# Optimization experiments

Hardware: AMD Instinct MI355X
Metric: run time of the kernel (lower is better)

## Reference

```python
import jax, jax.numpy as jnp
import numpy as np

TAU = 0.5

def _projection(z, W1, b1, W2, b2):
    h = jax.nn.elu(z @ W1.T + b1)
    return h @ W2.T + b2

def _normalize(x, eps=1e-12):
    n = jnp.linalg.norm(x, axis=1, keepdims=True)
    return x / jnp.maximum(n, eps)

def setup_inputs() -> dict:
    key = jax.random.key(0)
    k = jax.random.split(key, 6)
    N, D, P = 8192, 256, 256
    s = 1.0 / np.sqrt(D)
    return {
        "z1": jax.random.normal(k[0], (N, D), jnp.float32),
        "z2": jax.random.normal(k[1], (N, D), jnp.float32),
        "W1": jax.random.normal(k[2], (P, D), jnp.float32) * s,
        "b1": jnp.zeros((P,), jnp.float32),
        "W2": jax.random.normal(k[3], (D, P), jnp.float32) * s,
        "b2": jnp.zeros((D,), jnp.float32),
    }

def reference(z1, z2, W1, b1, W2, b2):
    h1 = _projection(z1, W1, b1, W2, b2)
    h2 = _projection(z2, W1, b1, W2, b2)
    n1 = _normalize(h1)
    n2 = _normalize(h2)
    f11 = jnp.exp((n1 @ n1.T) / TAU)  # [N,N]
    f22 = jnp.exp((n2 @ n2.T) / TAU)
    f12 = jnp.exp((n1 @ n2.T) / TAU)
    d12 = jnp.diagonal(f12)
    l1 = -jnp.log(d12 / (f11.sum(1) + f12.sum(1) - jnp.diagonal(f11)))
    # sim(h2,h1) = f12.T: diag same, row-sum = column-sum of f12
    l2 = -jnp.log(d12 / (f22.sum(1) + f12.sum(0) - jnp.diagonal(f22)))
    return (l1 + l2) * 0.5
```

## Files before the change

kernel.cpp:

```cpp
#include <hip/hip_runtime.h>
#include <hip/hip_bf16.h>
#include <hip/hip_fp8.h>
#include <stdint.h>

#define Nn 8192
#define TWO_N 16384
#define INV_TAU 2.0f

typedef unsigned short u16;
typedef unsigned char u8;
typedef __bf16 bf16x8 __attribute__((ext_vector_type(8)));
typedef float f32x4 __attribute__((ext_vector_type(4)));
typedef int i32x8 __attribute__((ext_vector_type(8)));

typedef const __attribute__((address_space(1))) void* gas_ptr;
typedef __attribute__((address_space(3))) void* las_ptr;

__device__ __forceinline__ void async_copy16(const void* g, void* l) {
  __builtin_amdgcn_global_load_lds((gas_ptr)g, (las_ptr)l, 16, 0, 0);
}

__global__ __launch_bounds__(256)
void mlp_norm(const float* __restrict__ z1, const float* __restrict__ z2,
              const float* __restrict__ W1, const float* __restrict__ b1,
              const float* __restrict__ W2, const float* __restrict__ b2,
              u8* __restrict__ Mf8, float* __restrict__ snorm,
              float* __restrict__ rsum) {
  __shared__ __bf16 sZ[64 * 64];
  __shared__ __bf16 sW[256 * 64];
  __shared__ __bf16 sH[64 * 256];
  const int bx = blockIdx.x;
  const int i0 = bx * 64;
  const float* Zsrc = (bx < 128) ? (z1 + (size_t)i0 * 256)
                                 : (z2 + (size_t)(i0 - Nn) * 256);
  const int t = threadIdx.x;
  const int lane = t & 63, wave = t >> 6;
  const int wn = wave * 64;
  const int fr = lane >> 4, fc = lane & 15;
  const int sw = fc & 7;

  if (t < 64) rsum[i0 + t] = 0.f;

  f32x4 acc[4][4];
#pragma unroll
  for (int a = 0; a < 4; a++)
#pragma unroll
    for (int b = 0; b < 4; b++) acc[a][b] = (f32x4){0.f, 0.f, 0.f, 0.f};

  for (int k0 = 0; k0 < 256; k0 += 64) {
    __syncthreads();
#pragma unroll
    for (int it = 0; it < 2; ++it) {
      int c = t + 256 * it;
      int row = c >> 3, g = (c & 7) ^ (row & 7);
      const float* s = Zsrc + (size_t)row * 256 + k0 + g * 8;
      float4 a0 = *(const float4*)s, a1 = *(const float4*)(s + 4);
      bf16x8 v = {(__bf16)a0.x, (__bf16)a0.y, (__bf16)a0.z, (__bf16)a0.w,
                  (__bf16)a1.x, (__bf16)a1.y, (__bf16)a1.z, (__bf16)a1.w};
      *(bf16x8*)&sZ[c * 8] = v;
    }
#pragma unroll
    for (int it = 0; it < 8; ++it) {
      int c = t + 256 * it;
      int row = c >> 3, g = (c & 7) ^ (row & 7);
      const float* s = W1 + (size_t)row * 256 + k0 + g * 8;
      float4 a0 = *(const float4*)s, a1 = *(const float4*)(s + 4);
      bf16x8 v = {(__bf16)a0.x, (__bf16)a0.y, (__bf16)a0.z, (__bf16)a0.w,
                  (__bf16)a1.x, (__bf16)a1.y, (__bf16)a1.z, (__bf16)a1.w};
      *(bf16x8*)&sW[c * 8] = v;
    }
    __syncthreads();
#pragma unroll
    for (int ks = 0; ks < 2; ++ks) {
      bf16x8 af[4], bfr[4];
#pragma unroll
      for (int mi = 0; mi < 4; mi++)
        af[mi] = *(const bf16x8*)&sZ[(mi * 16 + fc) * 64 + (((ks * 4 + fr) ^ sw) * 8)];
#pragma unroll
      for (int ni = 0; ni < 4; ni++)
        bfr[ni] = *(const bf16x8*)&sW[(wn + ni * 16 + fc) * 64 + (((ks * 4 + fr) ^ sw) * 8)];
#pragma unroll
      for (int mi = 0; mi < 4; mi++)
#pragma unroll
        for (int ni = 0; ni < 4; ni++)
          acc[mi][ni] = __builtin_amdgcn_mfma_f32_16x16x32_bf16(af[mi], bfr[ni], acc[mi][ni], 0, 0, 0);
    }
  }

  {
    float bv[4];
#pragma unroll
    for (int ni = 0; ni < 4; ni++) bv[ni] = b1[wn + ni * 16 + fc];
#pragma unroll
    for (int mi = 0; mi < 4; mi++)
#pragma unroll
      for (int ni = 0; ni < 4; ni++) {
        int col = wn + ni * 16 + fc;
        int gc = col >> 3;
#pragma unroll
        for (int r = 0; r < 4; r++) {
          int row = mi * 16 + fr * 4 + r;
          float v = acc[mi][ni][r] + bv[ni];
          v = v > 0.f ? v : (__expf(v) - 1.f);
          int pos = (gc & 24) | ((gc & 7) ^ (row & 7));
          sH[row * 256 + pos * 8 + (col & 7)] = (__bf16)v;
          acc[mi][ni][r] = 0.f;
        }
      }
  }

  for (int k0 = 0; k0 < 256; k0 += 64) {
    __syncthreads();
#pragma unroll
    for (int it = 0; it < 8; ++it) {
      int c = t + 256 * it;
      int row = c >> 3, g = (c & 7) ^ (row & 7);
      const float* s = W2 + (size_t)row * 256 + k0 + g * 8;
      float4 a0 = *(const float4*)s, a1 = *(const float4*)(s + 4);
      bf16x8 v = {(__bf16)a0.x, (__bf16)a0.y, (__bf16)a0.z, (__bf16)a0.w,
                  (__bf16)a1.x, (__bf16)a1.y, (__bf16)a1.z, (__bf16)a1.w};
      *(bf16x8*)&sW[c * 8] = v;
    }
    __syncthreads();
    const int kgb = k0 >> 3;
#pragma unroll
    for (int ks = 0; ks < 2; ++ks) {
      bf16x8 af[4], bfr[4];
#pragma unroll
      for (int mi = 0; mi < 4; mi++)
        af[mi] = *(const bf16x8*)&sH[(mi * 16 + fc) * 256 + (kgb + (((ks * 4 + fr) ^ sw))) * 8];
#pragma unroll
      for (int ni = 0; ni < 4; ni++)
        bfr[ni] = *(const bf16x8*)&sW[(wn + ni * 16 + fc) * 64 + (((ks * 4 + fr) ^ sw) * 8)];
#pragma unroll
      for (int mi = 0; mi < 4; mi++)
#pragma unroll
        for (int ni = 0; ni < 4; ni++)
          acc[mi][ni] = __builtin_amdgcn_mfma_f32_16x16x32_bf16(af[mi], bfr[ni], acc[mi][ni], 0, 0, 0);
    }
  }

  float bv[4];
#pragma unroll
  for (int ni = 0; ni < 4; ni++) bv[ni] = b2[wn + ni * 16 + fc];

  __syncthreads();
  float* red = (float*)sZ;
  float* red2 = red + 256;

#pragma unroll
  for (int mi = 0; mi < 4; mi++) {
    float ssq[4] = {0.f, 0.f, 0.f, 0.f};
#pragma unroll
    for (int ni = 0; ni < 4; ni++)
#pragma unroll
      for (int r = 0; r < 4; r++) {
        float v = acc[mi][ni][r] + bv[ni];
        acc[mi][ni][r] = v;
        ssq[r] += v * v;
      }
#pragma unroll
    for (int r = 0; r < 4; r++) {
      float v = ssq[r];
#pragma unroll
      for (int off = 1; off < 16; off <<= 1) v += __shfl_xor(v, off, 16);
      if (fc == 0) red[(mi * 16 + fr * 4 + r) * 4 + wave] = v;
    }
  }
  __syncthreads();

#pragma unroll
  for (int mi = 0; mi < 4; mi++) {
    float ssq2[4] = {0.f, 0.f, 0.f, 0.f};
#pragma unroll
    for (int r = 0; r < 4; r++) {
      int row = mi * 16 + fr * 4 + r;
      float ss = red[row * 4] + red[row * 4 + 1] + red[row * 4 + 2] + red[row * 4 + 3];
      float rn = 1.f / fmaxf(sqrtf(ss), 1e-12f);
#pragma unroll
      for (int ni = 0; ni < 4; ni++) {
        float v = acc[mi][ni][r] * rn;
        __hip_fp8_e4m3 q(v);
        Mf8[(size_t)(i0 + row) * 256 + wn + ni * 16 + fc] = q.__x;
        float fv = (float)q;
        ssq2[r] += fv * fv;
      }
    }
#pragma unroll
    for (int r = 0; r < 4; r++) {
      float v = ssq2[r];
#pragma unroll
      for (int off = 1; off < 16; off <<= 1) v += __shfl_xor(v, off, 16);
      if (fc == 0) red2[(mi * 16 + fr * 4 + r) * 4 + wave] = v;
    }
  }
  __syncthreads();
  if (t < 64)
    snorm[i0 + t] = red2[t * 4] + red2[t * 4 + 1] + red2[t * 4 + 2] + red2[t * 4 + 3];
}

__global__ __launch_bounds__(256, 2)
void gram_sym(const u8* __restrict__ Mf8, float* __restrict__ rsum) {
  __shared__ u8 sB8[2][128 * 256];
  const int t = threadIdx.x;
  const int lane = t & 63, wave = t >> 6;
  const int wm = (wave >> 1) * 64, wn = (wave & 1) * 64;
  const int fr = lane >> 4, fc = lane & 15;

  int f = 2111 - blockIdx.x;
  int b = 0;
  while (f >= 2 * (b + 1) * (b + 2)) ++b;
  int rem = f - 2 * b * (b + 1);
  int r = rem / (b + 1);
  int q = rem - r * (b + 1);
  int k = 4 * b + 1 + r;
  const int i_t = 128 - k;
  const int jt0 = i_t + 4 * q;
  const int L = min(4, k - 4 * q);
  const int i0 = i_t * 128;

  {
    const u8* Bg = Mf8 + (size_t)jt0 * 128 * 256;
#pragma unroll
    for (int it = 0; it < 8; ++it) {
      int c = t + 256 * it;
      int row = c >> 4, slot = c & 15;
      int g = slot ^ (row & 15);
      async_copy16(Bg + (size_t)row * 256 + g * 16, (void*)&sB8[0][c * 16]);
    }
  }

  i32x8 afr[4][2];
  {
    const u8* Ag = Mf8 + (size_t)i0 * 256;
#pragma unroll
    for (int mi = 0; mi < 4; ++mi) {
      const u8* rp = Ag + (size_t)(wm + mi * 16 + fc) * 256 + fr * 32;
#pragma unroll
      for (int kb = 0; kb < 2; ++kb) {
        int4 lo = *(const int4*)(rp + kb * 128);
        int4 hi = *(const int4*)(rp + kb * 128 + 16);
        afr[mi][kb] = (i32x8){lo.x, lo.y, lo.z, lo.w, hi.x, hi.y, hi.z, hi.w};
      }
    }
  }

  float rowacc[4][4];
#pragma unroll
  for (int a = 0; a < 4; a++)
#pragma unroll
    for (int rr = 0; rr < 4; rr++) rowacc[a][rr] = 0.f;

  for (int jt = 0; jt < L; ++jt) {
    const int j_t = jt0 + jt;
    const int j0 = j_t * 128;
    const u8* sB = &sB8[jt & 1][0];

    __syncthreads();

    if (jt + 1 < L) {
      const u8* Bg = Mf8 + (size_t)(j_t + 1) * 128 * 256;
      u8* dst = &sB8[(jt + 1) & 1][0];
#pragma unroll
      for (int it = 0; it < 8; ++it) {
        int c = t + 256 * it;
        int row = c >> 4, slot = c & 15;
        int g = slot ^ (row & 15);
        async_copy16(Bg + (size_t)row * 256 + g * 16, (void*)&dst[c * 16]);
      }
    }

    f32x4 acc[4][4];
#pragma unroll
    for (int a = 0; a < 4; a++)
#pragma unroll
      for (int bb = 0; bb < 4; bb++) acc[a][bb] = (f32x4){0.f, 0.f, 0.f, 0.f};

#pragma unroll
    for (int kb = 0; kb < 2; ++kb) {
      i32x8 bfrag[4];
#pragma unroll
      for (int ni = 0; ni < 4; ++ni) {
        const u8* base = sB + (wn + ni * 16 + fc) * 256;
        int g0 = kb * 8 + fr * 2;
        int4 lo = *(const int4*)(base + ((g0 ^ fc) * 16));
        int4 hi = *(const int4*)(base + (((g0 + 1) ^ fc) * 16));
        bfrag[ni] = (i32x8){lo.x, lo.y, lo.z, lo.w, hi.x, hi.y, hi.z, hi.w};
      }
#pragma unroll
      for (int mi = 0; mi < 4; mi++)
#pragma unroll
        for (int ni = 0; ni < 4; ni++)
          acc[mi][ni] = __builtin_amdgcn_mfma_scale_f32_16x16x128_f8f6f4(
              afr[mi][kb], bfrag[ni], acc[mi][ni], 0, 0, 0, 0x7F, 0, 0x7F);
    }

    float colp[4] = {0.f, 0.f, 0.f, 0.f};
#pragma unroll
    for (int mi = 0; mi < 4; mi++) {
#pragma unroll
      for (int ni = 0; ni < 4; ni++) {
        float e0 = __expf(acc[mi][ni][0] * INV_TAU);
        float e1 = __expf(acc[mi][ni][1] * INV_TAU);
        float e2 = __expf(acc[mi][ni][2] * INV_TAU);
        float e3 = __expf(acc[mi][ni][3] * INV_TAU);
        rowacc[mi][0] += e0; rowacc[mi][1] += e1;
        rowacc[mi][2] += e2; rowacc[mi][3] += e3;
        colp[ni] += e0 + e1 + e2 + e3;
      }
    }
    if (j_t != i_t) {
#pragma unroll
      for (int ni = 0; ni < 4; ni++) {
        float v = colp[ni];
        v += __shfl_xor(v, 16, 64);
        v += __shfl_xor(v, 32, 64);
        if (fr == 0) atomicAdd(&rsum[j0 + wn + ni * 16 + fc], v);
      }
    }
  }

#pragma unroll
  for (int mi = 0; mi < 4; mi++) {
#pragma unroll
    for (int rr = 0; rr < 4; rr++) {
      float v = rowacc[mi][rr];
#pragma unroll
      for (int off = 1; off < 16; off <<= 1) v += __shfl_xor(v, off, 16);
      rowacc[mi][rr] = v;
    }
  }
  if (fc == 0) {
#pragma unroll
    for (int mi = 0; mi < 4; mi++) {
      int rbase = i0 + wm + mi * 16 + fr * 4;
      atomicAdd(&rsum[rbase + 0], rowacc[mi][0]);
      atomicAdd(&rsum[rbase + 1], rowacc[mi][1]);
      atomicAdd(&rsum[rbase + 2], rowacc[mi][2]);
      atomicAdd(&rsum[rbase + 3], rowacc[mi][3]);
    }
  }
}

__global__ void final_loss(const u8* __restrict__ Mf8, const float* __restrict__ rsum,
                           const float* __restrict__ snorm, float* __restrict__ out) {
  int i = blockIdx.x * 4 + (threadIdx.x >> 6);
  int lane = threadIdx.x & 63;
  unsigned int ua = ((const unsigned int*)(Mf8 + (size_t)i * 256))[lane];
  unsigned int ub = ((const unsigned int*)(Mf8 + (size_t)(Nn + i) * 256))[lane];
  float d = 0.f;
#pragma unroll
  for (int e = 0; e < 4; ++e) {
    __hip_fp8_e4m3 qa, qb;
    qa.__x = (ua >> (8 * e)) & 0xFF;
    qb.__x = (ub >> (8 * e)) & 0xFF;
    d += (float)qa * (float)qb;
  }
#pragma unroll
  for (int off = 32; off; off >>= 1) d += __shfl_xor(d, off, 64);
  if (lane == 0) {
    float den1 = rsum[i] - __expf(snorm[i] * INV_TAU);
    float den2 = rsum[Nn + i] - __expf(snorm[Nn + i] * INV_TAU);
    out[i] = 0.5f * (logf(den1) + logf(den2)) - d * INV_TAU;
  }
}

extern "C" void kernel_launch(void* const* d_in, const int* in_sizes, int n_in,
                              void* d_out, int out_size, void* d_ws, size_t ws_size,
                              hipStream_t stream) {
  const float* z1 = (const float*)d_in[0];
  const float* z2 = (const float*)d_in[1];
  const float* W1 = (const float*)d_in[2];
  const float* b1 = (const float*)d_in[3];
  const float* W2 = (const float*)d_in[4];
  const float* b2 = (const float*)d_in[5];
  float* out = (float*)d_out;

  char* ws = (char*)d_ws;
  u8*    Mf8   = (u8*)(ws);
  float* rsum  = (float*)(ws + (4u << 20));
  float* snorm = (float*)(ws + (4u << 20) + 65536);

  mlp_norm<<<256, 256, 0, stream>>>(z1, z2, W1, b1, W2, b2, Mf8, snorm, rsum);

  gram_sym<<<2112, 256, 0, stream>>>(Mf8, rsum);

  final_loss<<<Nn / 4, 256, 0, stream>>>(Mf8, rsum, snorm, out);
}
```

Baseline: 176.7 us.

## Pre-cast weights to bf16, double-buffer MLP weight loads, halve gram LDS tiles

Adds a small kernel that converts W1/W2 to bf16 once per call, so mlp_norm can stream weights with async global-to-LDS copies into a double buffer and overlap them with MFMA work, including prefetching W2 during the last W1 chunk. In gram_sym, the B tile is split into two K-halves of 128 bytes each. This halves LDS per block and raises the launch-bounds occupancy hint from 2 to 4 blocks, while accumulators persist across the two halves. The cost is an extra kernel launch, more barriers per tile, and a different swizzle pattern.

After: 286.8 us. +62.3%, slower.

```diff
diff --git a/kernel.cpp b/kernel.cpp
--- a/kernel.cpp
+++ b/kernel.cpp
@@ -20,14 +20,31 @@
   __builtin_amdgcn_global_load_lds((gas_ptr)g, (las_ptr)l, 16, 0, 0);
 }
 
+__device__ __forceinline__ u16 f2bf(float x) {
+  uint32_t u = __float_as_uint(x);
+  u = u + 0x7fffu + ((u >> 16) & 1u);
+  return (u16)(u >> 16);
+}
+
+__global__ void wcast(const float* __restrict__ W1, const float* __restrict__ W2,
+                      u16* __restrict__ W1b, u16* __restrict__ W2b) {
+  int i = blockIdx.x * 256 + threadIdx.x;
+  float4 a = ((const float4*)W1)[i];
+  ushort4 o1; o1.x = f2bf(a.x); o1.y = f2bf(a.y); o1.z = f2bf(a.z); o1.w = f2bf(a.w);
+  ((ushort4*)W1b)[i] = o1;
+  float4 b = ((const float4*)W2)[i];
+  ushort4 o2; o2.x = f2bf(b.x); o2.y = f2bf(b.y); o2.z = f2bf(b.z); o2.w = f2bf(b.w);
+  ((ushort4*)W2b)[i] = o2;
+}
+
 __global__ __launch_bounds__(256)
 void mlp_norm(const float* __restrict__ z1, const float* __restrict__ z2,
-              const float* __restrict__ W1, const float* __restrict__ b1,
-              const float* __restrict__ W2, const float* __restrict__ b2,
+              const u16* __restrict__ W1b, const float* __restrict__ b1,
+              const u16* __restrict__ W2b, const float* __restrict__ b2,
               u8* __restrict__ Mf8, float* __restrict__ snorm,
               float* __restrict__ rsum) {
   __shared__ __bf16 sZ[64 * 64];
-  __shared__ __bf16 sW[256 * 64];
+  __shared__ __bf16 sW[2][256 * 64];
   __shared__ __bf16 sH[64 * 256];
   const int bx = blockIdx.x;
   const int i0 = bx * 64;
@@ -47,7 +64,15 @@
 #pragma unroll
     for (int b = 0; b < 4; b++) acc[a][b] = (f32x4){0.f, 0.f, 0.f, 0.f};
 
-  for (int k0 = 0; k0 < 256; k0 += 64) {
+#pragma unroll
+  for (int it = 0; it < 8; ++it) {
+    int c = t + 256 * it;
+    int row = c >> 3, g = (c & 7) ^ (row & 7);
+    async_copy16(W1b + (size_t)row * 256 + g * 8, (void*)&sW[0][c * 8]);
+  }
+
+  for (int cc = 0; cc < 4; ++cc) {
+    const int k0 = cc * 64;
     __syncthreads();
 #pragma unroll
     for (int it = 0; it < 2; ++it) {
@@ -59,17 +84,20 @@
                   (__bf16)a1.x, (__bf16)a1.y, (__bf16)a1.z, (__bf16)a1.w};
       *(bf16x8*)&sZ[c * 8] = v;
     }
-#pragma unroll
-    for (int it = 0; it < 8; ++it) {
-      int c = t + 256 * it;
-      int row = c >> 3, g = (c & 7) ^ (row & 7);
-      const float* s = W1 + (size_t)row * 256 + k0 + g * 8;
-      float4 a0 = *(const float4*)s, a1 = *(const float4*)(s + 4);
-      bf16x8 v = {(__bf16)a0.x, (__bf16)a0.y, (__bf16)a0.z, (__bf16)a0.w,
-                  (__bf16)a1.x, (__bf16)a1.y, (__bf16)a1.z, (__bf16)a1.w};
-      *(bf16x8*)&sW[c * 8] = v;
-    }
     __syncthreads();
+    {
+      int nc = cc + 1;
+      const u16* Wsrc = (nc < 4) ? W1b : W2b;
+      int nk0 = (nc & 3) * 64;
+      u16* dst = (u16*)&sW[nc & 1][0];
+#pragma unroll
+      for (int it = 0; it < 8; ++it) {
+        int c = t + 256 * it;
+        int row = c >> 3, g = (c & 7) ^ (row & 7);
+        async_copy16(Wsrc + (size_t)row * 256 + nk0 + g * 8, (void*)&dst[c * 8]);
+      }
+    }
+    const __bf16* sWc = &sW[cc & 1][0];
 #pragma unroll
     for (int ks = 0; ks < 2; ++ks) {
       bf16x8 af[4], bfr[4];
@@ -78,7 +106,7 @@
         af[mi] = *(const bf16x8*)&sZ[(mi * 16 + fc) * 64 + (((ks * 4 + fr) ^ sw) * 8)];
 #pragma unroll
       for (int ni = 0; ni < 4; ni++)
-        bfr[ni] = *(const bf16x8*)&sW[(wn + ni * 16 + fc) * 64 + (((ks * 4 + fr) ^ sw) * 8)];
+        bfr[ni] = *(const bf16x8*)&sWc[(wn + ni * 16 + fc) * 64 + (((ks * 4 + fr) ^ sw) * 8)];
 #pragma unroll
       for (int mi = 0; mi < 4; mi++)
 #pragma unroll
@@ -109,19 +137,21 @@
       }
   }
 
-  for (int k0 = 0; k0 < 256; k0 += 64) {
+  for (int cc = 4; cc < 8; ++cc) {
+    const int k0 = (cc & 3) * 64;
     __syncthreads();
-#pragma unroll
-    for (int it = 0; it < 8; ++it) {
-      int c = t + 256 * it;
-      int row = c >> 3, g = (c & 7) ^ (row & 7);
-      const float* s = W2 + (size_t)row * 256 + k0 + g * 8;
-      float4 a0 = *(const float4*)s, a1 = *(const float4*)(s + 4);
-      bf16x8 v = {(__bf16)a0.x, (__bf16)a0.y, (__bf16)a0.z, (__bf16)a0.w,
-                  (__bf16)a1.x, (__bf16)a1.y, (__bf16)a1.z, (__bf16)a1.w};
-      *(bf16x8*)&sW[c * 8] = v;
-    }
-    __syncthreads();
+    if (cc + 1 < 8) {
+      int nc = cc + 1;
+      int nk0 = (nc & 3) * 64;
+      u16* dst = (u16*)&sW[nc & 1][0];
+#pragma unroll
+      for (int it = 0; it < 8; ++it) {
+        int c = t + 256 * it;
+        int row = c >> 3, g = (c & 7) ^ (row & 7);
+        async_copy16(W2b + (size_t)row * 256 + nk0 + g * 8, (void*)&dst[c * 8]);
+      }
+    }
+    const __bf16* sWc = &sW[cc & 1][0];
     const int kgb = k0 >> 3;
 #pragma unroll
     for (int ks = 0; ks < 2; ++ks) {
@@ -131,7 +161,7 @@
         af[mi] = *(const bf16x8*)&sH[(mi * 16 + fc) * 256 + (kgb + (((ks * 4 + fr) ^ sw))) * 8];
 #pragma unroll
       for (int ni = 0; ni < 4; ni++)
-        bfr[ni] = *(const bf16x8*)&sW[(wn + ni * 16 + fc) * 64 + (((ks * 4 + fr) ^ sw) * 8)];
+        bfr[ni] = *(const bf16x8*)&sWc[(wn + ni * 16 + fc) * 64 + (((ks * 4 + fr) ^ sw) * 8)];
 #pragma unroll
       for (int mi = 0; mi < 4; mi++)
 #pragma unroll
@@ -199,9 +229,9 @@
     snorm[i0 + t] = red2[t * 4] + red2[t * 4 + 1] + red2[t * 4 + 2] + red2[t * 4 + 3];
 }
 
-__global__ __launch_bounds__(256, 2)
+__global__ __launch_bounds__(256, 4)
 void gram_sym(const u8* __restrict__ Mf8, float* __restrict__ rsum) {
-  __shared__ u8 sB8[2][128 * 256];
+  __shared__ u8 sB8[2][128 * 128];
   const int t = threadIdx.x;
   const int lane = t & 63, wave = t >> 6;
   const int wm = (wave >> 1) * 64, wn = (wave & 1) * 64;
@@ -222,10 +252,10 @@
   {
     const u8* Bg = Mf8 + (size_t)jt0 * 128 * 256;
 #pragma unroll
-    for (int it = 0; it < 8; ++it) {
+    for (int it = 0; it < 4; ++it) {
       int c = t + 256 * it;
-      int row = c >> 4, slot = c & 15;
-      int g = slot ^ (row & 15);
+      int row = c >> 3, slot = c & 7;
+      int g = slot ^ (row & 7);
       async_copy16(Bg + (size_t)row * 256 + g * 16, (void*)&sB8[0][c * 16]);
     }
   }
@@ -251,71 +281,73 @@
 #pragma unroll
     for (int rr = 0; rr < 4; rr++) rowacc[a][rr] = 0.f;
 
-  for (int jt = 0; jt < L; ++jt) {
-    const int j_t = jt0 + jt;
-    const int j0 = j_t * 128;
-    const u8* sB = &sB8[jt & 1][0];
-
+  f32x4 acc[4][4];
+#pragma unroll
+  for (int a = 0; a < 4; a++)
+#pragma unroll
+    for (int bb = 0; bb < 4; bb++) acc[a][bb] = (f32x4){0.f, 0.f, 0.f, 0.f};
+
+  const int totalc = L * 2;
+  for (int cc = 0; cc < totalc; ++cc) {
     __syncthreads();
 
-    if (jt + 1 < L) {
-      const u8* Bg = Mf8 + (size_t)(j_t + 1) * 128 * 256;
-      u8* dst = &sB8[(jt + 1) & 1][0];
-#pragma unroll
-      for (int it = 0; it < 8; ++it) {
+    if (cc + 1 < totalc) {
+      int nc = cc + 1;
+      const u8* Bg = Mf8 + (size_t)(jt0 + (nc >> 1)) * 128 * 256 + (nc & 1) * 128;
+      u8* dst = &sB8[nc & 1][0];
+#pragma unroll
+      for (int it = 0; it < 4; ++it) {
         int c = t + 256 * it;
-        int row = c >> 4, slot = c & 15;
-        int g = slot ^ (row & 15);
+        int row = c >> 3, slot = c & 7;
+        int g = slot ^ (row & 7);
         async_copy16(Bg + (size_t)row * 256 + g * 16, (void*)&dst[c * 16]);
       }
     }
 
-    f32x4 acc[4][4];
-#pragma unroll
-    for (int a = 0; a < 4; a++)
-#pragma unroll
-      for (int bb = 0; bb < 4; bb++) acc[a][bb] = (f32x4){0.f, 0.f, 0.f, 0.f};
-
-#pragma unroll
-    for (int kb = 0; kb < 2; ++kb) {
-      i32x8 bfrag[4];
-#pragma unroll
-      for (int ni = 0; ni < 4; ++ni) {
-        const u8* base = sB + (wn + ni * 16 + fc) * 256;
-        int g0 = kb * 8 + fr * 2;
-        int4 lo = *(const int4*)(base + ((g0 ^ fc) * 16));
-        int4 hi = *(const int4*)(base + (((g0 + 1) ^ fc) * 16));
-        bfrag[ni] = (i32x8){lo.x, lo.y, lo.z, lo.w, hi.x, hi.y, hi.z, hi.w};
-      }
-#pragma unroll
-      for (int mi = 0; mi < 4; mi++)
-#pragma unroll
-        for (int ni = 0; ni < 4; ni++)
-          acc[mi][ni] = __builtin_amdgcn_mfma_scale_f32_16x16x128_f8f6f4(
-              afr[mi][kb], bfrag[ni], acc[mi][ni], 0, 0, 0, 0x7F, 0, 0x7F);
-    }
-
-    float colp[4] = {0.f, 0.f, 0.f, 0.f};
-#pragma unroll
-    for (int mi = 0; mi < 4; mi++) {
-#pragma unroll
-      for (int ni = 0; ni < 4; ni++) {
-        float e0 = __expf(acc[mi][ni][0] * INV_TAU);
-        float e1 = __expf(acc[mi][ni][1] * INV_TAU);
-        float e2 = __expf(acc[mi][ni][2] * INV_TAU);
-        float e3 = __expf(acc[mi][ni][3] * INV_TAU);
-        rowacc[mi][0] += e0; rowacc[mi][1] += e1;
-        rowacc[mi][2] += e2; rowacc[mi][3] += e3;
-        colp[ni] += e0 + e1 + e2 + e3;
-      }
-    }
-    if (j_t != i_t) {
-#pragma unroll
-      for (int ni = 0; ni < 4; ni++) {
-        float v = colp[ni];
-        v += __shfl_xor(v, 16, 64);
-        v += __shfl_xor(v, 32, 64);
-        if (fr == 0) atomicAdd(&rsum[j0 + wn + ni * 16 + fc], v);
+    const int kb = cc & 1;
+    const u8* sB = &sB8[kb][0];
+    i32x8 bfrag[4];
+#pragma unroll
+    for (int ni = 0; ni < 4; ++ni) {
+      const u8* base = sB + (wn + ni * 16 + fc) * 128;
+      int g0 = fr * 2;
+      int4 lo = *(const int4*)(base + ((g0 ^ (fc & 7)) * 16));
+      int4 hi = *(const int4*)(base + (((g0 + 1) ^ (fc & 7)) * 16));
+      bfrag[ni] = (i32x8){lo.x, lo.y, lo.z, lo.w, hi.x, hi.y, hi.z, hi.w};
+    }
+#pragma unroll
+    for (int mi = 0; mi < 4; mi++)
+#pragma unroll
+      for (int ni = 0; ni < 4; ni++)
+        acc[mi][ni] = __builtin_amdgcn_mfma_scale_f32_16x16x128_f8f6f4(
+            afr[mi][kb], bfrag[ni], acc[mi][ni], 0, 0, 0, 0x7F, 0, 0x7F);
+
+    if (kb == 1) {
+      const int j_t = jt0 + (cc >> 1);
+      const int j0 = j_t * 128;
+      float colp[4] = {0.f, 0.f, 0.f, 0.f};
+#pragma unroll
+      for (int mi = 0; mi < 4; mi++) {
+#pragma unroll
+        for (int ni = 0; ni < 4; ni++) {
+          float e0 = __expf(acc[mi][ni][0] * INV_TAU);
+          float e1 = __expf(acc[mi][ni][1] * INV_TAU);
+          float e2 = __expf(acc[mi][ni][2] * INV_TAU);
+          float e3 = __expf(acc[mi][ni][3] * INV_TAU);
+          rowacc[mi][0] += e0; rowacc[mi][1] += e1;
+          rowacc[mi][2] += e2; rowacc[mi][3] += e3;
+          colp[ni] += e0 + e1 + e2 + e3;
+          acc[mi][ni] = (f32x4){0.f, 0.f, 0.f, 0.f};
+        }
+      }
+      if (j_t != i_t) {
+#pragma unroll
+        for (int ni = 0; ni < 4; ni++) {
+          float v = colp[ni];
+          v += __shfl_xor(v, 16, 64);
+          v += __shfl_xor(v, 32, 64);
+          if (fr == 0) atomicAdd(&rsum[j0 + wn + ni * 16 + fc], v);
+        }
       }
     }
   }
@@ -378,10 +410,14 @@
 
   char* ws = (char*)d_ws;
   u8*    Mf8   = (u8*)(ws);
-  float* rsum  = (float*)(ws + (4u << 20));
-  float* snorm = (float*)(ws + (4u << 20) + 65536);
-
-  mlp_norm<<<256, 256, 0, stream>>>(z1, z2, W1, b1, W2, b2, Mf8, snorm, rsum);
+  u16*   W1b   = (u16*)(ws + (4u << 20));
+  u16*   W2b   = (u16*)(ws + (4u << 20) + 131072);
+  float* rsum  = (float*)(ws + (4u << 20) + 262144);
+  float* snorm = (float*)(ws + (4u << 20) + 262144 + 65536);
+
+  wcast<<<64, 256, 0, stream>>>(W1, W2, W1b, W2b);
+
+  mlp_norm<<<256, 256, 0, stream>>>(z1, z2, W1b, b1, W2b, b2, Mf8, snorm, rsum);
 
   gram_sym<<<2112, 256, 0, stream>>>(Mf8, rsum);
 
```

## Split gram tiles into single-wave blocks loading B fragments directly from global

Applied to the files above, without the earlier changes.

The symmetric Gram kernel drops the shared-memory double-buffered B tile and its block barrier. Each 4-wave block becomes four single-wave blocks, one per 64x64 quadrant, and each wave reads its B fragments straight from global memory (L2/L1). This removes LDS staging and syncs and allows more, smaller blocks for scheduling. In exchange, B rows are fetched twice as often from cache rather than shared once through LDS, and the loads are no longer overlapped with compute by async prefetch.

After: 189.4 us. +7.1%, slower.

```diff
diff --git a/kernel.cpp b/kernel.cpp
--- a/kernel.cpp
+++ b/kernel.cpp
@@ -199,15 +199,15 @@
     snorm[i0 + t] = red2[t * 4] + red2[t * 4 + 1] + red2[t * 4 + 2] + red2[t * 4 + 3];
 }
 
-__global__ __launch_bounds__(256, 2)
+__global__ __launch_bounds__(64)
 void gram_sym(const u8* __restrict__ Mf8, float* __restrict__ rsum) {
-  __shared__ u8 sB8[2][128 * 256];
   const int t = threadIdx.x;
-  const int lane = t & 63, wave = t >> 6;
-  const int wm = (wave >> 1) * 64, wn = (wave & 1) * 64;
-  const int fr = lane >> 4, fc = lane & 15;
-
-  int f = 2111 - blockIdx.x;
+  const int fr = t >> 4, fc = t & 15;
+  const int strip = blockIdx.x >> 2;
+  const int role = blockIdx.x & 3;
+  const int wm = (role >> 1) * 64, wn = (role & 1) * 64;
+
+  int f = 2111 - strip;
   int b = 0;
   while (f >= 2 * (b + 1) * (b + 2)) ++b;
   int rem = f - 2 * b * (b + 1);
@@ -219,17 +219,6 @@
   const int L = min(4, k - 4 * q);
   const int i0 = i_t * 128;
 
-  {
-    const u8* Bg = Mf8 + (size_t)jt0 * 128 * 256;
-#pragma unroll
-    for (int it = 0; it < 8; ++it) {
-      int c = t + 256 * it;
-      int row = c >> 4, slot = c & 15;
-      int g = slot ^ (row & 15);
-      async_copy16(Bg + (size_t)row * 256 + g * 16, (void*)&sB8[0][c * 16]);
-    }
-  }
-
   i32x8 afr[4][2];
   {
     const u8* Ag = Mf8 + (size_t)i0 * 256;
@@ -254,21 +243,7 @@
   for (int jt = 0; jt < L; ++jt) {
     const int j_t = jt0 + jt;
     const int j0 = j_t * 128;
-    const u8* sB = &sB8[jt & 1][0];
-
-    __syncthreads();
-
-    if (jt + 1 < L) {
-      const u8* Bg = Mf8 + (size_t)(j_t + 1) * 128 * 256;
-      u8* dst = &sB8[(jt + 1) & 1][0];
-#pragma unroll
-      for (int it = 0; it < 8; ++it) {
-        int c = t + 256 * it;
-        int row = c >> 4, slot = c & 15;
-        int g = slot ^ (row & 15);
-        async_copy16(Bg + (size_t)row * 256 + g * 16, (void*)&dst[c * 16]);
-      }
-    }
+    const u8* Bg = Mf8 + (size_t)(j0 + wn) * 256 + fr * 32;
 
     f32x4 acc[4][4];
 #pragma unroll
@@ -281,10 +256,9 @@
       i32x8 bfrag[4];
 #pragma unroll
       for (int ni = 0; ni < 4; ++ni) {
-        const u8* base = sB + (wn + ni * 16 + fc) * 256;
-        int g0 = kb * 8 + fr * 2;
-        int4 lo = *(const int4*)(base + ((g0 ^ fc) * 16));
-        int4 hi = *(const int4*)(base + (((g0 + 1) ^ fc) * 16));
+        const u8* rp = Bg + (size_t)(ni * 16 + fc) * 256 + kb * 128;
+        int4 lo = *(const int4*)rp;
+        int4 hi = *(const int4*)(rp + 16);
         bfrag[ni] = (i32x8){lo.x, lo.y, lo.z, lo.w, hi.x, hi.y, hi.z, hi.w};
       }
 #pragma unroll
@@ -383,7 +357,7 @@
 
   mlp_norm<<<256, 256, 0, stream>>>(z1, z2, W1, b1, W2, b2, Mf8, snorm, rsum);
 
-  gram_sym<<<2112, 256, 0, stream>>>(Mf8, rsum);
+  gram_sym<<<2112 * 4, 64, 0, stream>>>(Mf8, rsum);
 
   final_loss<<<Nn / 4, 256, 0, stream>>>(Mf8, rsum, snorm, out);
 }
```
